# Performance work log

Hardware: AMD Instinct MI355X
Metric: run time of the kernel (lower is better)

The kernel has to match this reference:

```python
import jax, jax.numpy as jnp
import numpy as np

B, Q, KV = 4, 256, 1024
QS, KS, H, VS = 128, 128, 128, 256

def setup_inputs() -> dict:
    key = jax.random.key(0)
    ks = jax.random.split(key, 7)
    return {
        "queries": jax.random.normal(ks[0], (B, Q, QS), dtype=jnp.float32),
        "keys": jax.random.normal(ks[1], (B, KV, KS), dtype=jnp.float32),
        "values": jax.random.normal(ks[2], (B, KV, VS), dtype=jnp.float32),
        "valid_lens": jax.random.randint(ks[3], (B,), 0, KV, dtype=jnp.int64 if jax.config.read('jax_enable_x64') else jnp.int32),
        "Wq": jax.random.normal(ks[4], (QS, H), dtype=jnp.float32),
        "Wk": jax.random.normal(ks[5], (KS, H), dtype=jnp.float32),
        "wv": jax.random.normal(ks[6], (H,), dtype=jnp.float32),
    }

def reference(queries, keys, values, valid_lens, Wq, Wk, wv):
    # project: [B,Q,H], [B,KV,H]
    q = jnp.einsum('bqd,dh->bqh', queries, Wq)
    k = jnp.einsum('bkd,dh->bkh', keys, Wk)
    # additive scores: broadcast add -> tanh -> reduce with w_v  [B,Q,KV]
    feats = jnp.tanh(q[:, :, None, :] + k[:, None, :, :])  # [B,Q,KV,H]
    scores = jnp.einsum('bqkh,h->bqk', feats, wv)
    # masked softmax over KV with value -1e6 at masked slots
    mask = jnp.arange(scores.shape[-1])[None, None, :] < valid_lens[:, None, None]
    scores = jnp.where(mask, scores, -1e6)
    attn = jax.nn.softmax(scores, axis=-1)
    # weighted sum of values  [B,Q,VS]
    return jnp.einsum('bqk,bkv->bqv', attn, values)
```

## Files before the change

kernel.cpp:

```cpp
#include <hip/hip_runtime.h>

#define LOG2E   1.4426950408889634f

typedef _Float16 fh2 __attribute__((ext_vector_type(2)));
typedef __fp16   ph2 __attribute__((ext_vector_type(2)));
typedef float    f32x2 __attribute__((ext_vector_type(2)));
union h2u { fh2 f; ph2 p; unsigned int u; };
__device__ __forceinline__ unsigned int pk2bits(ph2 h) { h2u t; t.p = h; return t.u; }
__device__ __forceinline__ fh2 pk2f(ph2 h) { h2u t; t.p = h; return t.f; }
__device__ __forceinline__ fh2 bits2f(unsigned int u) { h2u t; t.u = u; return t.f; }

__global__ __launch_bounds__(256) void proj_kernel(
    const float* __restrict__ q_in, const float* __restrict__ k_in,
    const float* __restrict__ v_in,
    const float* __restrict__ Wq, const float* __restrict__ Wk,
    const int* __restrict__ valid_lens,
    float* __restrict__ qc, float* __restrict__ kct,
    unsigned int* __restrict__ vh)
{
    __shared__ __align__(16) float x_s[8][128];
    __shared__ __align__(16) float ps[4][8][128];
    int tid = threadIdx.x;
    int blk = blockIdx.x;

    if (blk >= 640) {
        int vb = blk - 640;
        int P  = vb*4 + (tid >> 6);
        int bb = P >> 9, p = P & 511;
        int lane = tid & 63;
        const float4* r0 = (const float4*)(v_in + ((size_t)(bb*1024 + 2*p))*256) + lane;
        float4 x0 = r0[0];
        float4 x1 = r0[64];
        uint4 h;
        h.x = pk2bits(__builtin_amdgcn_cvt_pkrtz(x0.x, x1.x));
        h.y = pk2bits(__builtin_amdgcn_cvt_pkrtz(x0.y, x1.y));
        h.z = pk2bits(__builtin_amdgcn_cvt_pkrtz(x0.z, x1.z));
        h.w = pk2bits(__builtin_amdgcn_cvt_pkrtz(x0.w, x1.w));
        ((uint4*)vh)[(size_t)P*64 + lane] = h;
        return;
    }

    bool is_q = (blk < 128);
    int r0 = (is_q ? blk : blk - 128) * 8;
    int bb = r0 >> 10;
    if (!is_q) {
        int vl = valid_lens[bb];
        if ((r0 & 1023) >= vl) return;
    }
    const float* X = (is_q ? q_in : k_in) + (size_t)r0 * 128;
    const float* W = is_q ? Wq : Wk;

    *(float4*)&x_s[tid >> 5][(tid & 31) * 4] = ((const float4*)X)[tid];
    __syncthreads();

    int hl = tid & 63;
    int dq = tid >> 6;
    float a0[8] = {0,0,0,0,0,0,0,0};
    float a1[8] = {0,0,0,0,0,0,0,0};
#pragma unroll
    for (int i4 = 0; i4 < 8; ++i4) {
        int d = dq*32 + i4*4;
        float w00 = W[(d+0)*128 + hl], w01 = W[(d+0)*128 + hl + 64];
        float w10 = W[(d+1)*128 + hl], w11 = W[(d+1)*128 + hl + 64];
        float w20 = W[(d+2)*128 + hl], w21 = W[(d+2)*128 + hl + 64];
        float w30 = W[(d+3)*128 + hl], w31 = W[(d+3)*128 + hl + 64];
#pragma unroll
        for (int r = 0; r < 8; ++r) {
            float4 xv = *(const float4*)&x_s[r][d];
            a0[r] = fmaf(xv.x,w00, fmaf(xv.y,w10, fmaf(xv.z,w20, fmaf(xv.w,w30, a0[r]))));
            a1[r] = fmaf(xv.x,w01, fmaf(xv.y,w11, fmaf(xv.z,w21, fmaf(xv.w,w31, a1[r]))));
        }
    }
#pragma unroll
    for (int r = 0; r < 8; ++r) {
        ps[dq][r][hl]      = a0[r];
        ps[dq][r][hl + 64] = a1[r];
    }
    __syncthreads();

    int r  = tid >> 5;
    int c4 = (tid & 31) * 4;
    float4 s0 = *(const float4*)&ps[0][r][c4];
    float4 s1 = *(const float4*)&ps[1][r][c4];
    float4 s2 = *(const float4*)&ps[2][r][c4];
    float4 s3 = *(const float4*)&ps[3][r][c4];
    float4 v;
    v.x = __builtin_amdgcn_exp2f(((s0.x+s1.x)+(s2.x+s3.x))*LOG2E);
    v.y = __builtin_amdgcn_exp2f(((s0.y+s1.y)+(s2.y+s3.y))*LOG2E);
    v.z = __builtin_amdgcn_exp2f(((s0.z+s1.z)+(s2.z+s3.z))*LOG2E);
    v.w = __builtin_amdgcn_exp2f(((s0.w+s1.w)+(s2.w+s3.w))*LOG2E);
    if (is_q) {
        *(float4*)&qc[(size_t)(r0 + r)*128 + c4] = v;
    } else {
        int c    = (r0 & 1023) >> 6;
        int kvin = (r0 & 63) + r;
        *(float4*)&kct[((((size_t)(bb*16 + c))*32 + (c4 >> 2))*64 + kvin)*4] = v;
    }
}

__global__ __launch_bounds__(512, 8) void attn_split_kernel(
    const float* __restrict__ qc, const float* __restrict__ kct,
    const unsigned int* __restrict__ vh, const int* __restrict__ valid_lens,
    const float* __restrict__ wv, float* __restrict__ pO, float* __restrict__ pml)
{
    __shared__ __align__(16) float2 e2_s[512];
    __shared__ float4 po[8][2][64];
    __shared__ float2 red_m[8], red_s[8];

    int tid  = threadIdx.x;
    int b    = blockIdx.y;
    int q0   = blockIdx.x * 2;
    int s    = blockIdx.z;
    int w    = tid >> 6;
    int lane = tid & 63;
    int vl   = valid_lens[b];
    int row0 = b*256 + q0;

    if (s == 1 && vl > 0 && vl <= 512) {
        if (tid < 2) pml[(size_t)(1024 + row0 + tid)*2] = -1e30f;
        return;
    }

    const float4* qa4 = (const float4*)(qc + (size_t)row0*128);
    const float4* qb4 = qa4 + 32;
    const float4* wv4 = (const float4*)wv;
    const float4* p0  = (const float4*)kct + ((size_t)(b*16 + s*8 + w))*2048 + lane;

    const f32x2 one2 = {1.f, 1.f};
    f32x2 acc0 = {0.f, 0.f}, acc1 = {0.f, 0.f};
    if ((s*8 + w)*64 < vl) {
#pragma unroll 4
        for (int hb = 0; hb < 32; ++hb) {
            float4 wvv = wv4[hb];
            float4 qa = qa4[hb], qb = qb4[hb];
            float4 k0 = p0[(size_t)hb*64];
            const f32x2* w2  = (const f32x2*)&wvv;
            const f32x2* qa2 = (const f32x2*)&qa;
            const f32x2* qb2 = (const f32x2*)&qb;
            const f32x2* k2  = (const f32x2*)&k0;
#pragma unroll
            for (int h = 0; h < 2; ++h) {
                f32x2 t0 = qa2[h] * k2[h];
                f32x2 t1 = qb2[h] * k2[h];
                f32x2 d0 = t0*t0 + one2;
                f32x2 d1 = t1*t1 + one2;
                f32x2 r0 = { __builtin_amdgcn_rcpf(d0.x), __builtin_amdgcn_rcpf(d0.y) };
                f32x2 r1 = { __builtin_amdgcn_rcpf(d1.x), __builtin_amdgcn_rcpf(d1.y) };
                acc0 += w2[h] * r0;
                acc1 += w2[h] * r1;
            }
        }
    }
    float a00 = acc0.x + acc0.y;
    float a10 = acc1.x + acc1.y;

    int lkv = w*64 + lane;
    bool valid = (s*512 + lkv < vl);
    float s00 = valid ? -2.f*a00 : -1e6f;
    float s10 = valid ? -2.f*a10 : -1e6f;

    float m0 = s00, m1 = s10;
#pragma unroll
    for (int off = 32; off; off >>= 1) {
        m0 = fmaxf(m0, __shfl_xor(m0, off));
        m1 = fmaxf(m1, __shfl_xor(m1, off));
    }
    if (lane == 0) red_m[w] = make_float2(m0, m1);
    __syncthreads();
    {
        float2 mm = red_m[0];
#pragma unroll
        for (int ww = 1; ww < 8; ++ww) {
            float2 t = red_m[ww];
            mm.x = fmaxf(mm.x, t.x); mm.y = fmaxf(mm.y, t.y);
        }
        m0 = mm.x; m1 = mm.y;
    }

    float e00 = __builtin_amdgcn_exp2f((s00 - m0) * LOG2E);
    float e10 = __builtin_amdgcn_exp2f((s10 - m1) * LOG2E);
    e2_s[lkv] = make_float2(e00, e10);
    float l0 = e00, l1 = e10;
#pragma unroll
    for (int off = 32; off; off >>= 1) {
        l0 += __shfl_xor(l0, off);
        l1 += __shfl_xor(l1, off);
    }
    if (lane == 0) red_s[w] = make_float2(l0, l1);
    __syncthreads();

    int local_end = (vl == 0) ? 512 : min(512, vl - s*512);
    int pair_end  = (local_end + 1) >> 1;
    float4 ac0 = {0,0,0,0}, ac1 = {0,0,0,0};
    const uint4* VH = (const uint4*)vh + ((size_t)b*512 + (size_t)s*256)*64 + lane;
#pragma unroll 2
    for (int p = w; p < pair_end; p += 8) {
        uint4 vv = VH[(size_t)p*64];
        float4 E = *(const float4*)&e2_s[2*p];
        fh2 eh0 = pk2f(__builtin_amdgcn_cvt_pkrtz(E.x, E.z));
        fh2 eh1 = pk2f(__builtin_amdgcn_cvt_pkrtz(E.y, E.w));
        fh2 v0 = bits2f(vv.x), v1 = bits2f(vv.y);
        fh2 v2 = bits2f(vv.z), v3 = bits2f(vv.w);
        ac0.x = __builtin_amdgcn_fdot2(eh0, v0, ac0.x, false);
        ac0.y = __builtin_amdgcn_fdot2(eh0, v1, ac0.y, false);
        ac0.z = __builtin_amdgcn_fdot2(eh0, v2, ac0.z, false);
        ac0.w = __builtin_amdgcn_fdot2(eh0, v3, ac0.w, false);
        ac1.x = __builtin_amdgcn_fdot2(eh1, v0, ac1.x, false);
        ac1.y = __builtin_amdgcn_fdot2(eh1, v1, ac1.y, false);
        ac1.z = __builtin_amdgcn_fdot2(eh1, v2, ac1.z, false);
        ac1.w = __builtin_amdgcn_fdot2(eh1, v3, ac1.w, false);
    }
    po[w][0][lane] = ac0;
    po[w][1][lane] = ac1;

    if (tid < 2) {
        float lsum = 0.f;
#pragma unroll
        for (int ww = 0; ww < 8; ++ww) {
            float2 t = red_s[ww];
            lsum += tid ? t.y : t.x;
        }
        float mm = tid ? m1 : m0;
        *(float2*)&pml[(size_t)(s*1024 + row0 + tid)*2] = make_float2(mm, lsum);
    }
    __syncthreads();

    int qq  = tid >> 8;
    int col = tid & 255;
    const float* pp = (const float*)po;
    float r = 0.f;
#pragma unroll
    for (int ww = 0; ww < 8; ++ww) r += pp[(ww*2 + qq)*256 + col];
    pO[(size_t)(s*1024 + row0 + qq)*256 + col] = r;
}

__global__ __launch_bounds__(256) void combine_kernel(
    const float* __restrict__ pO, const float* __restrict__ pml,
    float* __restrict__ out)
{
    int tid  = threadIdx.x;
    int row  = blockIdx.x*4 + (tid >> 6);
    int lane = tid & 63;
    float2 ml0 = *(const float2*)&pml[(size_t)row*2];
    float2 ml1 = *(const float2*)&pml[(size_t)(1024 + row)*2];
    float m  = fmaxf(ml0.x, ml1.x);
    float w0 = __builtin_amdgcn_exp2f((ml0.x - m) * LOG2E);
    float w1 = __builtin_amdgcn_exp2f((ml1.x - m) * LOG2E);
    float inv = 1.0f / (w0*ml0.y + w1*ml1.y);
    float4 o0 = ((const float4*)pO)[(size_t)row*64 + lane];
    float4 o1 = ((const float4*)pO)[(size_t)(1024 + row)*64 + lane];
    float4 o;
    o.x = (w0*o0.x + w1*o1.x) * inv;
    o.y = (w0*o0.y + w1*o1.y) * inv;
    o.z = (w0*o0.z + w1*o1.z) * inv;
    o.w = (w0*o0.w + w1*o1.w) * inv;
    ((float4*)out)[(size_t)row*64 + lane] = o;
}

extern "C" void kernel_launch(void* const* d_in, const int* in_sizes, int n_in,
                              void* d_out, int out_size, void* d_ws, size_t ws_size,
                              hipStream_t stream)
{
    const float* queries = (const float*)d_in[0];
    const float* keys    = (const float*)d_in[1];
    const float* values  = (const float*)d_in[2];
    const int*   vlens   = (const int*)d_in[3];
    const float* Wq      = (const float*)d_in[4];
    const float* Wk      = (const float*)d_in[5];
    const float* wv      = (const float*)d_in[6];
    float* out = (float*)d_out;

    float* qc  = (float*)d_ws;
    float* kct = qc  + 4*256*128;
    float* pO  = kct + 4*16*32*64*4;
    float* pml = pO  + 2*1024*256;
    unsigned int* vh = (unsigned int*)(pml + 2*1024*2);

    proj_kernel<<<1152, 256, 0, stream>>>(queries, keys, values, Wq, Wk, vlens, qc, kct, vh);
    attn_split_kernel<<<dim3(128, 4, 2), 512, 0, stream>>>(qc, kct, vh, vlens, wv, pO, pml);
    combine_kernel<<<256, 256, 0, stream>>>(pO, pml, out);
}
```

Baseline: 88.36 us.

## Process four query rows per block and split KV into four 256-wide chunks

Attention blocks now handle four query rows each, with 256 threads covering a 256-wide KV chunk, and the grid splits KV four ways. Each key load and rcp chain is shared across twice as many query rows, and value loads are reused for four rows. Chunks beyond valid_len exit early. The cost is more partial-output traffic to combine, four-way merge work, and extra syncs for the two-pass reduction of po, plus higher register pressure.

```diff
diff --git a/kernel.cpp b/kernel.cpp
--- a/kernel.cpp
+++ b/kernel.cpp
@@ -98,107 +98,127 @@
     }
 }
 
-__global__ __launch_bounds__(512, 8) void attn_split_kernel(
+__global__ __launch_bounds__(256, 8) void attn_split_kernel(
     const float* __restrict__ qc, const float* __restrict__ kct,
     const unsigned int* __restrict__ vh, const int* __restrict__ valid_lens,
     const float* __restrict__ wv, float* __restrict__ pO, float* __restrict__ pml)
 {
-    __shared__ __align__(16) float2 e2_s[512];
-    __shared__ float4 po[8][2][64];
-    __shared__ float2 red_m[8], red_s[8];
+    __shared__ __align__(16) float4 e4_s[256];
+    __shared__ float4 po[4][2][64];
+    __shared__ float4 red_m[4], red_s[4];
 
     int tid  = threadIdx.x;
     int b    = blockIdx.y;
-    int q0   = blockIdx.x * 2;
+    int q0   = blockIdx.x * 4;
     int s    = blockIdx.z;
     int w    = tid >> 6;
     int lane = tid & 63;
     int vl   = valid_lens[b];
     int row0 = b*256 + q0;
 
-    if (s == 1 && vl > 0 && vl <= 512) {
-        if (tid < 2) pml[(size_t)(1024 + row0 + tid)*2] = -1e30f;
+    if (s > 0 && vl > 0 && s*256 >= vl) {
+        if (tid < 4) *(float2*)&pml[(size_t)(s*1024 + row0 + tid)*2] = make_float2(-1e30f, 0.f);
         return;
     }
 
-    const float4* qa4 = (const float4*)(qc + (size_t)row0*128);
-    const float4* qb4 = qa4 + 32;
+    const float4* qr0 = (const float4*)(qc + (size_t)row0*128);
+    const float4* qr1 = qr0 + 32;
+    const float4* qr2 = qr0 + 64;
+    const float4* qr3 = qr0 + 96;
     const float4* wv4 = (const float4*)wv;
-    const float4* p0  = (const float4*)kct + ((size_t)(b*16 + s*8 + w))*2048 + lane;
+    int chunk = s*4 + w;
+    const float4* p0  = (const float4*)kct + ((size_t)(b*16 + chunk))*2048 + lane;
 
     const f32x2 one2 = {1.f, 1.f};
-    f32x2 acc0 = {0.f, 0.f}, acc1 = {0.f, 0.f};
-    if ((s*8 + w)*64 < vl) {
-#pragma unroll 4
+    f32x2 acc0 = {0.f,0.f}, acc1 = {0.f,0.f}, acc2 = {0.f,0.f}, acc3 = {0.f,0.f};
+
+#define ROWOP(xq, accv) { \
+        f32x2 t = ((const f32x2*)&(xq))[h] * kk; \
+        f32x2 d = t*t + one2; \
+        f32x2 rv = { __builtin_amdgcn_rcpf(d.x), __builtin_amdgcn_rcpf(d.y) }; \
+        accv += ww * rv; }
+
+    if (chunk*64 < vl) {
+#pragma unroll 2
         for (int hb = 0; hb < 32; ++hb) {
+            float4 k0 = p0[(size_t)hb*64];
             float4 wvv = wv4[hb];
-            float4 qa = qa4[hb], qb = qb4[hb];
-            float4 k0 = p0[(size_t)hb*64];
-            const f32x2* w2  = (const f32x2*)&wvv;
-            const f32x2* qa2 = (const f32x2*)&qa;
-            const f32x2* qb2 = (const f32x2*)&qb;
-            const f32x2* k2  = (const f32x2*)&k0;
+            float4 xa = qr0[hb], xb = qr1[hb], xc = qr2[hb], xd = qr3[hb];
+            const f32x2* k2 = (const f32x2*)&k0;
+            const f32x2* w2 = (const f32x2*)&wvv;
 #pragma unroll
             for (int h = 0; h < 2; ++h) {
-                f32x2 t0 = qa2[h] * k2[h];
-                f32x2 t1 = qb2[h] * k2[h];
-                f32x2 d0 = t0*t0 + one2;
-                f32x2 d1 = t1*t1 + one2;
-                f32x2 r0 = { __builtin_amdgcn_rcpf(d0.x), __builtin_amdgcn_rcpf(d0.y) };
-                f32x2 r1 = { __builtin_amdgcn_rcpf(d1.x), __builtin_amdgcn_rcpf(d1.y) };
-                acc0 += w2[h] * r0;
-                acc1 += w2[h] * r1;
+                f32x2 kk = k2[h];
+                f32x2 ww = w2[h];
+                ROWOP(xa, acc0);
+                ROWOP(xb, acc1);
+                ROWOP(xc, acc2);
+                ROWOP(xd, acc3);
             }
         }
     }
-    float a00 = acc0.x + acc0.y;
-    float a10 = acc1.x + acc1.y;
+#undef ROWOP
+    float a0 = acc0.x + acc0.y;
+    float a1 = acc1.x + acc1.y;
+    float a2 = acc2.x + acc2.y;
+    float a3 = acc3.x + acc3.y;
 
     int lkv = w*64 + lane;
-    bool valid = (s*512 + lkv < vl);
-    float s00 = valid ? -2.f*a00 : -1e6f;
-    float s10 = valid ? -2.f*a10 : -1e6f;
-
-    float m0 = s00, m1 = s10;
+    bool valid = (s*256 + lkv < vl);
+    float s0 = valid ? -2.f*a0 : -1e6f;
+    float s1 = valid ? -2.f*a1 : -1e6f;
+    float s2 = valid ? -2.f*a2 : -1e6f;
+    float s3 = valid ? -2.f*a3 : -1e6f;
+
+    float m0 = s0, m1 = s1, m2 = s2, m3 = s3;
 #pragma unroll
     for (int off = 32; off; off >>= 1) {
         m0 = fmaxf(m0, __shfl_xor(m0, off));
         m1 = fmaxf(m1, __shfl_xor(m1, off));
-    }
-    if (lane == 0) red_m[w] = make_float2(m0, m1);
+        m2 = fmaxf(m2, __shfl_xor(m2, off));
+        m3 = fmaxf(m3, __shfl_xor(m3, off));
+    }
+    if (lane == 0) red_m[w] = make_float4(m0, m1, m2, m3);
     __syncthreads();
     {
-        float2 mm = red_m[0];
-#pragma unroll
-        for (int ww = 1; ww < 8; ++ww) {
-            float2 t = red_m[ww];
+        float4 mm = red_m[0];
+#pragma unroll
+        for (int ww2 = 1; ww2 < 4; ++ww2) {
+            float4 t = red_m[ww2];
             mm.x = fmaxf(mm.x, t.x); mm.y = fmaxf(mm.y, t.y);
-        }
-        m0 = mm.x; m1 = mm.y;
-    }
-
-    float e00 = __builtin_amdgcn_exp2f((s00 - m0) * LOG2E);
-    float e10 = __builtin_amdgcn_exp2f((s10 - m1) * LOG2E);
-    e2_s[lkv] = make_float2(e00, e10);
-    float l0 = e00, l1 = e10;
+            mm.z = fmaxf(mm.z, t.z); mm.w = fmaxf(mm.w, t.w);
+        }
+        m0 = mm.x; m1 = mm.y; m2 = mm.z; m3 = mm.w;
+    }
+
+    float e0 = __builtin_amdgcn_exp2f((s0 - m0) * LOG2E);
+    float e1 = __builtin_amdgcn_exp2f((s1 - m1) * LOG2E);
+    float e2 = __builtin_amdgcn_exp2f((s2 - m2) * LOG2E);
+    float e3 = __builtin_amdgcn_exp2f((s3 - m3) * LOG2E);
+    e4_s[lkv] = make_float4(e0, e1, e2, e3);
+    float l0 = e0, l1 = e1, l2 = e2, l3 = e3;
 #pragma unroll
     for (int off = 32; off; off >>= 1) {
         l0 += __shfl_xor(l0, off);
         l1 += __shfl_xor(l1, off);
-    }
-    if (lane == 0) red_s[w] = make_float2(l0, l1);
-    __syncthreads();
-
-    int local_end = (vl == 0) ? 512 : min(512, vl - s*512);
+        l2 += __shfl_xor(l2, off);
+        l3 += __shfl_xor(l3, off);
+    }
+    if (lane == 0) red_s[w] = make_float4(l0, l1, l2, l3);
+    __syncthreads();
+
+    int local_end = (vl == 0) ? 256 : min(256, vl - s*256);
     int pair_end  = (local_end + 1) >> 1;
-    float4 ac0 = {0,0,0,0}, ac1 = {0,0,0,0};
-    const uint4* VH = (const uint4*)vh + ((size_t)b*512 + (size_t)s*256)*64 + lane;
+    float4 ac0 = {0,0,0,0}, ac1 = {0,0,0,0}, ac2 = {0,0,0,0}, ac3 = {0,0,0,0};
+    const uint4* VH = (const uint4*)vh + ((size_t)(b*512 + s*128))*64 + lane;
 #pragma unroll 2
-    for (int p = w; p < pair_end; p += 8) {
+    for (int p = w; p < pair_end; p += 4) {
         uint4 vv = VH[(size_t)p*64];
-        float4 E = *(const float4*)&e2_s[2*p];
-        fh2 eh0 = pk2f(__builtin_amdgcn_cvt_pkrtz(E.x, E.z));
-        fh2 eh1 = pk2f(__builtin_amdgcn_cvt_pkrtz(E.y, E.w));
+        float4 E0 = e4_s[2*p], E1 = e4_s[2*p+1];
+        fh2 eh0 = pk2f(__builtin_amdgcn_cvt_pkrtz(E0.x, E1.x));
+        fh2 eh1 = pk2f(__builtin_amdgcn_cvt_pkrtz(E0.y, E1.y));
+        fh2 eh2 = pk2f(__builtin_amdgcn_cvt_pkrtz(E0.z, E1.z));
+        fh2 eh3 = pk2f(__builtin_amdgcn_cvt_pkrtz(E0.w, E1.w));
         fh2 v0 = bits2f(vv.x), v1 = bits2f(vv.y);
         fh2 v2 = bits2f(vv.z), v3 = bits2f(vv.w);
         ac0.x = __builtin_amdgcn_fdot2(eh0, v0, ac0.x, false);
@@ -209,29 +229,56 @@
         ac1.y = __builtin_amdgcn_fdot2(eh1, v1, ac1.y, false);
         ac1.z = __builtin_amdgcn_fdot2(eh1, v2, ac1.z, false);
         ac1.w = __builtin_amdgcn_fdot2(eh1, v3, ac1.w, false);
-    }
+        ac2.x = __builtin_amdgcn_fdot2(eh2, v0, ac2.x, false);
+        ac2.y = __builtin_amdgcn_fdot2(eh2, v1, ac2.y, false);
+        ac2.z = __builtin_amdgcn_fdot2(eh2, v2, ac2.z, false);
+        ac2.w = __builtin_amdgcn_fdot2(eh2, v3, ac2.w, false);
+        ac3.x = __builtin_amdgcn_fdot2(eh3, v0, ac3.x, false);
+        ac3.y = __builtin_amdgcn_fdot2(eh3, v1, ac3.y, false);
+        ac3.z = __builtin_amdgcn_fdot2(eh3, v2, ac3.z, false);
+        ac3.w = __builtin_amdgcn_fdot2(eh3, v3, ac3.w, false);
+    }
+
+    if (tid < 4) {
+        float lsum = 0.f;
+#pragma unroll
+        for (int ww2 = 0; ww2 < 4; ++ww2) {
+            float4 t = red_s[ww2];
+            lsum += (tid == 0) ? t.x : (tid == 1) ? t.y : (tid == 2) ? t.z : t.w;
+        }
+        float mm = (tid == 0) ? m0 : (tid == 1) ? m1 : (tid == 2) ? m2 : m3;
+        *(float2*)&pml[(size_t)(s*1024 + row0 + tid)*2] = make_float2(mm, lsum);
+    }
+
+    int qq = tid >> 7;
+    int cp = tid & 127;
+    const float2* pp2 = (const float2*)po;
+
     po[w][0][lane] = ac0;
     po[w][1][lane] = ac1;
-
-    if (tid < 2) {
-        float lsum = 0.f;
-#pragma unroll
-        for (int ww = 0; ww < 8; ++ww) {
-            float2 t = red_s[ww];
-            lsum += tid ? t.y : t.x;
-        }
-        float mm = tid ? m1 : m0;
-        *(float2*)&pml[(size_t)(s*1024 + row0 + tid)*2] = make_float2(mm, lsum);
-    }
-    __syncthreads();
-
-    int qq  = tid >> 8;
-    int col = tid & 255;
-    const float* pp = (const float*)po;
-    float r = 0.f;
-#pragma unroll
-    for (int ww = 0; ww < 8; ++ww) r += pp[(ww*2 + qq)*256 + col];
-    pO[(size_t)(s*1024 + row0 + qq)*256 + col] = r;
+    __syncthreads();
+    {
+        float2 r = make_float2(0.f, 0.f);
+#pragma unroll
+        for (int ww2 = 0; ww2 < 4; ++ww2) {
+            float2 t = pp2[(ww2*2 + qq)*128 + cp];
+            r.x += t.x; r.y += t.y;
+        }
+        *(float2*)&pO[(size_t)(s*1024 + row0 + qq)*256 + cp*2] = r;
+    }
+    __syncthreads();
+    po[w][0][lane] = ac2;
+    po[w][1][lane] = ac3;
+    __syncthreads();
+    {
+        float2 r = make_float2(0.f, 0.f);
+#pragma unroll
+        for (int ww2 = 0; ww2 < 4; ++ww2) {
+            float2 t = pp2[(ww2*2 + qq)*128 + cp];
+            r.x += t.x; r.y += t.y;
+        }
+        *(float2*)&pO[(size_t)(s*1024 + row0 + 2 + qq)*256 + cp*2] = r;
+    }
 }
 
 __global__ __launch_bounds__(256) void combine_kernel(
@@ -243,17 +290,23 @@
     int lane = tid & 63;
     float2 ml0 = *(const float2*)&pml[(size_t)row*2];
     float2 ml1 = *(const float2*)&pml[(size_t)(1024 + row)*2];
-    float m  = fmaxf(ml0.x, ml1.x);
+    float2 ml2 = *(const float2*)&pml[(size_t)(2048 + row)*2];
+    float2 ml3 = *(const float2*)&pml[(size_t)(3072 + row)*2];
+    float m  = fmaxf(fmaxf(ml0.x, ml1.x), fmaxf(ml2.x, ml3.x));
     float w0 = __builtin_amdgcn_exp2f((ml0.x - m) * LOG2E);
     float w1 = __builtin_amdgcn_exp2f((ml1.x - m) * LOG2E);
-    float inv = 1.0f / (w0*ml0.y + w1*ml1.y);
+    float w2 = __builtin_amdgcn_exp2f((ml2.x - m) * LOG2E);
+    float w3 = __builtin_amdgcn_exp2f((ml3.x - m) * LOG2E);
+    float inv = 1.0f / (w0*ml0.y + w1*ml1.y + w2*ml2.y + w3*ml3.y);
     float4 o0 = ((const float4*)pO)[(size_t)row*64 + lane];
     float4 o1 = ((const float4*)pO)[(size_t)(1024 + row)*64 + lane];
+    float4 o2 = ((const float4*)pO)[(size_t)(2048 + row)*64 + lane];
+    float4 o3 = ((const float4*)pO)[(size_t)(3072 + row)*64 + lane];
     float4 o;
-    o.x = (w0*o0.x + w1*o1.x) * inv;
-    o.y = (w0*o0.y + w1*o1.y) * inv;
-    o.z = (w0*o0.z + w1*o1.z) * inv;
-    o.w = (w0*o0.w + w1*o1.w) * inv;
+    o.x = (w0*o0.x + w1*o1.x + w2*o2.x + w3*o3.x) * inv;
+    o.y = (w0*o0.y + w1*o1.y + w2*o2.y + w3*o3.y) * inv;
+    o.z = (w0*o0.z + w1*o1.z + w2*o2.z + w3*o3.z) * inv;
+    o.w = (w0*o0.w + w1*o1.w + w2*o2.w + w3*o3.w) * inv;
     ((float4*)out)[(size_t)row*64 + lane] = o;
 }
 
@@ -273,10 +326,10 @@
     float* qc  = (float*)d_ws;
     float* kct = qc  + 4*256*128;
     float* pO  = kct + 4*16*32*64*4;
-    float* pml = pO  + 2*1024*256;
-    unsigned int* vh = (unsigned int*)(pml + 2*1024*2);
+    float* pml = pO  + 4*1024*256;
+    unsigned int* vh = (unsigned int*)(pml + 4*1024*2);
 
     proj_kernel<<<1152, 256, 0, stream>>>(queries, keys, values, Wq, Wk, vlens, qc, kct, vh);
-    attn_split_kernel<<<dim3(128, 4, 2), 512, 0, stream>>>(qc, kct, vh, vlens, wv, pO, pml);
+    attn_split_kernel<<<dim3(64, 4, 4), 256, 0, stream>>>(qc, kct, vh, vlens, wv, pO, pml);
     combine_kernel<<<256, 256, 0, stream>>>(pO, pml, out);
 }
```

After: 92.85 us. +5.1%, slower.
